# Optimization experiments

Measured on AMD Instinct MI355X. Metric: run time of the kernel, lower is better.

The kernel has to match this reference:

```python
import jax, jax.numpy as jnp
from jax import lax
import numpy as np

VOCAB, EMB, HID = 32000, 512, 512
START, STOP = 1, 2
B, T = 32, 32


def setup_inputs() -> dict:
    key = jax.random.key(0)
    ks = jax.random.split(key, 9)
    s = 0.02
    return {
        "x": jax.random.normal(ks[0], (B, HID), jnp.float32),
        "labels": jax.random.randint(ks[1], (B, T), 0, VOCAB),
        "coin": jax.random.randint(ks[2], (B, T), 0, 2).astype(bool),
        "emb": jax.random.normal(ks[3], (VOCAB, EMB), jnp.float32) * s,
        "Wi": jax.random.normal(ks[4], (EMB, 4 * HID), jnp.float32) * s,
        "Wh": jax.random.normal(ks[5], (HID, 4 * HID), jnp.float32) * s,
        "b": jnp.zeros((4 * HID,), jnp.float32),
        "Wo": jax.random.normal(ks[6], (HID, VOCAB), jnp.float32) * s,
        "bo": jnp.zeros((VOCAB,), jnp.float32),
    }


def reference(x, labels, coin, emb, Wi, Wh, b, Wo, bo):
    Bsz, Tlen = labels.shape

    def cell(inp, hn, cn):
        # PyTorch LSTMCell gate order: i, f, g, o
        gates = inp @ Wi + hn @ Wh + b  # [B, 4H]
        i_, f_, g_, o_ = jnp.split(gates, 4, axis=-1)
        cn = jax.nn.sigmoid(f_) * cn + jax.nn.sigmoid(i_) * jnp.tanh(g_)
        hn = jax.nn.sigmoid(o_) * jnp.tanh(cn)
        out = hn @ Wo + bo  # [B, V] logits
        return out, hn, cn

    inp0 = jnp.broadcast_to(emb[START], (Bsz, emb.shape[1]))
    hn0 = x                       # init_states: hidden <- image feature
    cn0 = jnp.zeros_like(x)
    loss0 = jnp.zeros((), jnp.float32)

    def step(carry, t_in):
        inp, hn, cn, loss = carry
        label_t, coin_t = t_in    # [B], [B]
        out, hn, cn = cell(inp, hn, cn)
        logp = jax.nn.log_softmax(out, axis=-1)
        ce = -jnp.take_along_axis(logp, label_t[:, None], axis=1)[:, 0]
        loss = loss + ce.sum()
        pred = jnp.argmax(out, axis=-1)  # scheduled sampling
        next_tok = jnp.where(coin_t, pred, label_t)
        return (emb[next_tok], hn, cn, loss), None

    (inp, hn, cn, loss), _ = lax.scan(step, (inp0, hn0, cn0, loss0), (labels.T, coin.T))

    # final STOP step
    out, hn, cn = cell(inp, hn, cn)
    logp = jax.nn.log_softmax(out, axis=-1)
    loss = loss + (-logp[:, STOP]).sum()
    return loss / Bsz
```

## Files before the change

kernel.cpp:

```cpp
#include <hip/hip_runtime.h>
#include <math.h>

#define VOCABSZ 32000
#define EMBD 512
#define HIDD 512
#define BSZ 32
#define TLEN 32
#define G4 2048
#define NGRP 1000
#define NLB 250
#define PSTRIDE 8192
#define SW 256.0f
#define SH 16.0f
#define INV_SWH (1.0f / (SW * SH))

using bf16x8 = __attribute__((ext_vector_type(8))) short;
using f32x16 = __attribute__((ext_vector_type(16))) float;
typedef long long i64;

__device__ __forceinline__ float sigmoidf_(float x) { return 1.f / (1.f + expf(-x)); }
__device__ __forceinline__ unsigned short f2bf(float f) {
    unsigned u = __float_as_uint(f);
    return (unsigned short)((u + 0x7fffu + ((u >> 16) & 1u)) >> 16);
}
__device__ __forceinline__ unsigned char f2e4m3(float f) {
    unsigned u = __float_as_uint(f);
    unsigned s = (u >> 24) & 0x80u;
    int e = (int)((u >> 23) & 0xffu);
    unsigned m = u & 0x7fffffu;
    int ee = e - 120;
    if (ee >= 16) return (unsigned char)(s | 0x7E);
    if (ee <= 0) return (unsigned char)s;
    unsigned r = m + 0x7FFFFu + ((m >> 20) & 1u);
    if (r & 0x800000u) { ee += 1; r = 0; if (ee >= 16) return (unsigned char)(s | 0x7E); }
    unsigned mant = (r >> 20) & 7u;
    if (ee == 15 && mant == 7u) return (unsigned char)(s | 0x7E);
    return (unsigned char)(s | (unsigned)(ee << 3) | mant);
}

__global__ void init6_kernel(const float* __restrict__ x,
                             const void* __restrict__ coin,
                             float* __restrict__ cst,
                             unsigned short* __restrict__ hbf,
                             unsigned char* __restrict__ hf8,
                             float* __restrict__ ce_acc, int* __restrict__ flag) {
    __shared__ int s_f;
    int tid = threadIdx.x;
    if (tid == 0) s_f = 0;
    __syncthreads();
    if (tid < 256 && ((const unsigned int*)coin)[tid] > 1u) s_f = 1;
    __syncthreads();
    if (tid == 0) *flag = s_f;
    if (tid < 32) ce_acc[tid] = 0.f;
    for (int i = tid; i < BSZ * HIDD; i += blockDim.x) {
        float v = x[i];
        cst[i] = 0.f;
        hbf[i] = f2bf(v);
        hf8[i] = f2e4m3(v * SH);
    }
}

__global__ __launch_bounds__(256) void emb_prep_kernel(
    const float* __restrict__ emb, unsigned short* __restrict__ embbf) {
    size_t i8 = ((size_t)blockIdx.x * 256 + threadIdx.x) * 8;
    float4 a = *(const float4*)&emb[i8];
    float4 b = *(const float4*)&emb[i8 + 4];
    bf16x8 v;
    v[0] = (short)f2bf(a.x); v[1] = (short)f2bf(a.y);
    v[2] = (short)f2bf(a.z); v[3] = (short)f2bf(a.w);
    v[4] = (short)f2bf(b.x); v[5] = (short)f2bf(b.y);
    v[6] = (short)f2bf(b.z); v[7] = (short)f2bf(b.w);
    *(bf16x8*)&embbf[i8] = v;
}

__global__ __launch_bounds__(256) void wot8_prep_kernel(
    const float* __restrict__ Wo, i64* __restrict__ wot8) {
    __shared__ unsigned char s[512 * 32];
    int g = blockIdx.x;
    int tid = threadIdx.x;
    int col = tid & 31;
    int k0 = tid >> 5;
    for (int kk = k0; kk < 512; kk += 8)
        s[kk * 32 + col] = f2e4m3(Wo[(size_t)kk * VOCABSZ + g * 32 + col] * SW);
    __syncthreads();
    for (int f = tid; f < 2048; f += 256) {
        int kt = f >> 6, lane = f & 63;
        int kb = kt * 16 + ((lane >> 5) << 3);
        int c = lane & 31;
        union { unsigned char b[8]; i64 v; } u;
        #pragma unroll
        for (int j = 0; j < 8; ++j) u.b[j] = s[(kb + j) * 32 + c];
        wot8[(size_t)g * 2048 + f] = u.v;
    }
}

__global__ __launch_bounds__(256) void wcell_prep_kernel(
    const float* __restrict__ Wi, const float* __restrict__ Wh,
    unsigned short* __restrict__ wcell) {
    __shared__ unsigned short s[512 * 32];
    int cb = blockIdx.x >> 1;
    int half = blockIdx.x & 1;
    const float* Wsrc = half ? Wh : Wi;
    int tid = threadIdx.x;
    int lc = tid & 31;
    int gcol = (lc >> 3) * 512 + cb * 8 + (lc & 7);
    int k0 = tid >> 5;
    for (int kl = k0; kl < 512; kl += 8)
        s[kl * 32 + lc] = f2bf(Wsrc[(size_t)kl * G4 + gcol]);
    __syncthreads();
    bf16x8* out8 = (bf16x8*)wcell;
    for (int f = tid; f < 2048; f += 256) {
        int ktl = f >> 6, lane = f & 63;
        int kb = ktl * 16 + ((lane >> 5) << 3);
        int c = lane & 31;
        bf16x8 v;
        #pragma unroll
        for (int j = 0; j < 8; ++j) v[j] = (short)s[(kb + j) * 32 + c];
        out8[((size_t)cb * 64 + half * 32 + ktl) * 64 + lane] = v;
    }
}

__global__ __launch_bounds__(1024) void cell_mfma4_kernel(
    const float* __restrict__ emb, const unsigned short* __restrict__ embbf,
    const int* __restrict__ labels,
    const void* __restrict__ coin, const int* __restrict__ flag,
    const unsigned short* __restrict__ wcell, const float* __restrict__ bias,
    float* __restrict__ cst, unsigned short* __restrict__ hbf,
    unsigned char* __restrict__ hf8,
    const float* __restrict__ part, float* __restrict__ ce_acc, int t) {
    __shared__ float sg[16][32][32];
    __shared__ float st[32][33];
    __shared__ int s_tok[32];
    int tid = threadIdx.x;
    int cb = blockIdx.x;
    int lane = tid & 63, wv = tid >> 6;

    if (t == 0) {
        if (tid < 32) s_tok[tid] = 1;
    } else {
        int row = tid >> 5, slot = tid & 31;
        int tm1 = t - 1;
        float m = -3.0e38f; int mi = 0;
        for (int ib = slot; ib < NLB; ib += 32) {
            int e = row * 256 + ib;
            float pm = part[e];
            int pi = __float_as_int(part[2 * PSTRIDE + e]);
            if (pm > m || (pm == m && pi < mi)) { m = pm; mi = pi; }
        }
        #pragma unroll
        for (int d = 1; d < 32; d <<= 1) {
            float om = __shfl_xor(m, d);
            int omi = __shfl_xor(mi, d);
            if (om > m || (om == m && omi < mi)) { m = om; mi = omi; }
        }
        if (slot == 0) {
            int lab = labels[row * TLEN + tm1];
            int cn = (*flag) ? (int)((const unsigned char*)coin)[row * TLEN + tm1]
                             : ((const int*)coin)[row * TLEN + tm1];
            s_tok[row] = cn ? mi : lab;
        }
        if (cb == 0) {
            float M = -3.0e38f, S = 0.f, L = -INFINITY;
            for (int ib = slot; ib < NLB; ib += 32) {
                int e = row * 256 + ib;
                float pm = part[e], ps = part[PSTRIDE + e];
                float nM = fmaxf(M, pm);
                S = S * expf(M - nM) + ps * expf(pm - nM);
                M = nM;
                L = fmaxf(L, part[3 * PSTRIDE + e]);
            }
            #pragma unroll
            for (int d = 1; d < 32; d <<= 1) {
                float oM = __shfl_xor(M, d), oS = __shfl_xor(S, d);
                float nM = fmaxf(M, oM);
                S = S * expf(M - nM) + oS * expf(oM - nM);
                M = nM;
                L = fmaxf(L, __shfl_xor(L, d));
            }
            if (slot == 0) ce_acc[row] += (M + logf(S)) - L;
        }
    }
    __syncthreads();

    int r = lane & 31;
    int ksub = (lane >> 5) << 3;
    const bf16x8* wp = (const bf16x8*)wcell + ((size_t)cb * 64 + wv * 4) * 64 + lane;

    f32x16 acc = {};
    if (wv < 8) {
        int tok = s_tok[r];
        if (embbf) {
            const unsigned short* eb = embbf + (size_t)tok * EMBD;
            #pragma unroll
            for (int i = 0; i < 4; ++i) {
                int k = (wv * 4 + i) * 16 + ksub;
                bf16x8 a = *(const bf16x8*)&eb[k];
                acc = __builtin_amdgcn_mfma_f32_32x32x16_bf16(a, wp[i * 64], acc, 0, 0, 0);
            }
        } else {
            const float* ebase = emb + (size_t)tok * EMBD;
            #pragma unroll
            for (int i = 0; i < 4; ++i) {
                int k = (wv * 4 + i) * 16 + ksub;
                float4 e0 = *(const float4*)(ebase + k);
                float4 e1 = *(const float4*)(ebase + k + 4);
                bf16x8 a;
                a[0] = (short)f2bf(e0.x); a[1] = (short)f2bf(e0.y);
                a[2] = (short)f2bf(e0.z); a[3] = (short)f2bf(e0.w);
                a[4] = (short)f2bf(e1.x); a[5] = (short)f2bf(e1.y);
                a[6] = (short)f2bf(e1.z); a[7] = (short)f2bf(e1.w);
                acc = __builtin_amdgcn_mfma_f32_32x32x16_bf16(a, wp[i * 64], acc, 0, 0, 0);
            }
        }
    } else {
        #pragma unroll
        for (int i = 0; i < 4; ++i) {
            int k = (wv * 4 + i) * 16 + ksub - 512;
            bf16x8 a = *(const bf16x8*)&hbf[r * HIDD + k];
            acc = __builtin_amdgcn_mfma_f32_32x32x16_bf16(a, wp[i * 64], acc, 0, 0, 0);
        }
    }

    int half = lane >> 5;
    #pragma unroll
    for (int reg = 0; reg < 16; ++reg) {
        int row = (reg & 3) + 8 * (reg >> 2) + 4 * half;
        sg[wv][row][lane & 31] = acc[reg];
    }
    __syncthreads();

    {
        int row = tid >> 5, lc = tid & 31;
        float s = 0.f;
        #pragma unroll
        for (int w = 0; w < 16; ++w) s += sg[w][row][lc];
        st[row][lc] = s;
    }
    __syncthreads();

    if (tid < 256) {
        int rr = tid >> 3, jj = tid & 7;
        int jh = cb * 8 + jj;
        float i_ = bias[jh]        + st[rr][jj];
        float f_ = bias[jh + 512]  + st[rr][jj + 8];
        float g_ = bias[jh + 1024] + st[rr][jj + 16];
        float o_ = bias[jh + 1536] + st[rr][jj + 24];
        int idx = rr * HIDD + jh;
        float ci = cst[idx];
        float cn = sigmoidf_(f_) * ci + sigmoidf_(i_) * tanhf(g_);
        float hn = sigmoidf_(o_) * tanhf(cn);
        cst[idx] = cn;
        hbf[idx] = f2bf(hn);
        hf8[idx] = f2e4m3(hn * SH);
    }
}

__global__ __launch_bounds__(256) void logits_fp8_kernel(
    const i64* __restrict__ wot8, const unsigned char* __restrict__ h_f8,
    const float* __restrict__ bo, const int* __restrict__ labels,
    float* __restrict__ part, int t) {
    __shared__ __align__(16) i64 s_h[2048];
    __shared__ int s_lab[32];
    __shared__ float s_pm[4][32], s_ps[4][32], s_pl[4][32], s_pst[4][32];
    __shared__ int s_pi[4][32];
    int tid = threadIdx.x;
    int lane = tid & 63, wv = tid >> 6;

    for (int f = tid; f < 2048; f += 256) {
        int kt = f >> 6, ln = f & 63;
        int row = ln & 31, kb = kt * 16 + ((ln >> 5) << 3);
        s_h[f] = *(const i64*)&h_f8[row * 512 + kb];
    }
    if (tid < 32) s_lab[tid] = labels[tid * TLEN + t];
    __syncthreads();

    int g = blockIdx.x * 4 + wv;
    const i64* wp = wot8 + (size_t)g * 2048 + lane;

    f32x16 acc0 = {}, acc1 = {};
    #pragma unroll 4
    for (int kt = 0; kt < 16; ++kt) {
        acc0 = __builtin_amdgcn_mfma_f32_32x32x16_fp8_fp8(
            s_h[kt * 64 + lane], wp[kt * 64], acc0, 0, 0, 0);
        acc1 = __builtin_amdgcn_mfma_f32_32x32x16_fp8_fp8(
            s_h[(kt + 16) * 64 + lane], wp[(kt + 16) * 64], acc1, 0, 0, 0);
    }

    int half = lane >> 5;
    int colw = lane & 31;
    int col = g * 32 + colw;
    float bq = bo[col];

    #pragma unroll
    for (int reg = 0; reg < 16; ++reg) {
        int row = (reg & 3) + 8 * (reg >> 2) + 4 * half;
        float v = (acc0[reg] + acc1[reg]) * INV_SWH + bq;
        float m = v; int mi = col;
        #pragma unroll
        for (int d = 1; d < 32; d <<= 1) {
            float om = __shfl_xor(m, d);
            int omi = __shfl_xor(mi, d);
            if (om > m || (om == m && omi < mi)) { m = om; mi = omi; }
        }
        float e = expf(v - m), ssum = e;
        #pragma unroll
        for (int d = 1; d < 32; d <<= 1) ssum += __shfl_xor(ssum, d);
        int labc = s_lab[row];
        float lv = __shfl(v, (labc & 31) + (half << 5));
        if ((labc >> 5) != g) lv = -INFINITY;
        float sv = __shfl(v, 2 + (half << 5));
        if (g != 0) sv = -INFINITY;
        if (colw == 0) {
            s_pm[wv][row] = m; s_ps[wv][row] = ssum; s_pi[wv][row] = mi;
            s_pl[wv][row] = lv; s_pst[wv][row] = sv;
        }
    }
    __syncthreads();

    if (tid < 32) {
        int row = tid;
        float M = s_pm[0][row], S = s_ps[0][row];
        int MI = s_pi[0][row];
        float L = s_pl[0][row], ST = s_pst[0][row];
        #pragma unroll
        for (int w = 1; w < 4; ++w) {
            float pm = s_pm[w][row], ps = s_ps[w][row];
            int pi = s_pi[w][row];
            float nM = fmaxf(M, pm);
            S = S * expf(M - nM) + ps * expf(pm - nM);
            if (pm > M || (pm == M && pi < MI)) MI = pi;
            M = nM;
            L = fmaxf(L, s_pl[w][row]);
            ST = fmaxf(ST, s_pst[w][row]);
        }
        int e0 = row * 256 + blockIdx.x;
        part[e0] = M;
        part[PSTRIDE + e0] = S;
        part[2 * PSTRIDE + e0] = __int_as_float(MI);
        part[3 * PSTRIDE + e0] = L;
        part[4 * PSTRIDE + e0] = ST;
    }
}

__global__ __launch_bounds__(256) void finalize5_kernel(
    const float* __restrict__ part, const float* __restrict__ ce_acc,
    float* __restrict__ out) {
    __shared__ float s_ce[32];
    int tid = threadIdx.x;
    int row = tid >> 3, slot = tid & 7;
    float M = -3.0e38f, S = 0.f, ST = -INFINITY;
    for (int ib = slot; ib < NLB; ib += 8) {
        int e = row * 256 + ib;
        float pm = part[e], ps = part[PSTRIDE + e];
        float nM = fmaxf(M, pm);
        S = S * expf(M - nM) + ps * expf(pm - nM);
        M = nM;
        ST = fmaxf(ST, part[4 * PSTRIDE + e]);
    }
    #pragma unroll
    for (int d = 1; d < 8; d <<= 1) {
        float oM = __shfl_xor(M, d), oS = __shfl_xor(S, d);
        float nM = fmaxf(M, oM);
        S = S * expf(M - nM) + oS * expf(oM - nM);
        M = nM;
        ST = fmaxf(ST, __shfl_xor(ST, d));
    }
    if (slot == 0) s_ce[row] = ce_acc[row] + (M + logf(S)) - ST;
    __syncthreads();
    if (tid == 0) {
        float tot = 0.f;
        for (int r = 0; r < 32; ++r) tot += s_ce[r];
        *out = tot / 32.f;
    }
}

extern "C" void kernel_launch(void* const* d_in, const int* in_sizes, int n_in,
                              void* d_out, int out_size, void* d_ws, size_t ws_size,
                              hipStream_t stream) {
    const float* x      = (const float*)d_in[0];
    const int*   labels = (const int*)  d_in[1];
    const void*  coin   =               d_in[2];
    const float* emb    = (const float*)d_in[3];
    const float* Wi     = (const float*)d_in[4];
    const float* Wh     = (const float*)d_in[5];
    const float* b      = (const float*)d_in[6];
    const float* Wo     = (const float*)d_in[7];
    const float* bo     = (const float*)d_in[8];

    float* ws     = (float*)d_ws;
    float* cst    = ws;
    unsigned short* h_bf = (unsigned short*)(ws + 16384);
    unsigned char*  h_f8 = (unsigned char*)(ws + 24576);
    float* part   = ws + 28672;
    float* ce_acc = ws + 69632;
    int*   flag   = (int*)(ws + 69664);
    unsigned short* wcell = (unsigned short*)(ws + 69696);
    i64*   wot8   = (i64*)(ws + 69696 + 1048576);
    unsigned short* embbf = (unsigned short*)(ws + 69696 + 1048576 + 4096000);
    float* outp   = (float*)d_out;

    size_t need_emb = (size_t)(69696 + 1048576 + 4096000 + 8192000) * 4;
    const unsigned short* embbf_use = (ws_size >= need_emb) ? embbf : (const unsigned short*)0;

    wot8_prep_kernel<<<NGRP, 256, 0, stream>>>(Wo, wot8);
    wcell_prep_kernel<<<128, 256, 0, stream>>>(Wi, Wh, wcell);
    if (embbf_use)
        emb_prep_kernel<<<VOCABSZ * EMBD / 2048, 256, 0, stream>>>(emb, embbf);
    init6_kernel<<<1, 256, 0, stream>>>(x, coin, cst, h_bf, h_f8, ce_acc, flag);

    for (int t = 0; t < 33; ++t) {
        int tt = (t < 32) ? t : 0;
        cell_mfma4_kernel<<<64, 1024, 0, stream>>>(emb, embbf_use, labels, coin,
                                                   flag, wcell, b, cst, h_bf,
                                                   h_f8, part, ce_acc, t);
        logits_fp8_kernel<<<NLB, 256, 0, stream>>>(wot8, h_f8, bo, labels,
                                                   part, tt);
    }
    finalize5_kernel<<<1, 256, 0, stream>>>(part, ce_acc, outp);
}
```

Measured before the change: 1.234 ms.

## Split logits K-reduction across two waves with 16-byte interleaved FP8 loads

The logits kernel now runs 512 threads per block, and two waves cover each 32-column group by splitting the K dimension in half. Partial accumulators from the second half pass through shared memory before the softmax/argmax reduction. Weights and hidden states are re-laid out so each lane loads two consecutive k-tiles with a single 16-byte load. The init kernel is also spread over 64 blocks instead of one. The aim is more waves in flight to hide memory latency on the weight stream, at the cost of an extra LDS round-trip and barrier.

```diff
diff --git a/kernel.cpp b/kernel.cpp
--- a/kernel.cpp
+++ b/kernel.cpp
@@ -38,26 +38,26 @@
     return (unsigned char)(s | (unsigned)(ee << 3) | mant);
 }
 
-__global__ void init6_kernel(const float* __restrict__ x,
-                             const void* __restrict__ coin,
-                             float* __restrict__ cst,
-                             unsigned short* __restrict__ hbf,
-                             unsigned char* __restrict__ hf8,
-                             float* __restrict__ ce_acc, int* __restrict__ flag) {
+__global__ __launch_bounds__(256) void init7_kernel(
+    const float* __restrict__ x, const void* __restrict__ coin,
+    float* __restrict__ cst, unsigned short* __restrict__ hbf,
+    unsigned char* __restrict__ hf8,
+    float* __restrict__ ce_acc, int* __restrict__ flag) {
     __shared__ int s_f;
     int tid = threadIdx.x;
-    if (tid == 0) s_f = 0;
-    __syncthreads();
-    if (tid < 256 && ((const unsigned int*)coin)[tid] > 1u) s_f = 1;
-    __syncthreads();
-    if (tid == 0) *flag = s_f;
-    if (tid < 32) ce_acc[tid] = 0.f;
-    for (int i = tid; i < BSZ * HIDD; i += blockDim.x) {
-        float v = x[i];
-        cst[i] = 0.f;
-        hbf[i] = f2bf(v);
-        hf8[i] = f2e4m3(v * SH);
-    }
+    int i = blockIdx.x * 256 + tid;
+    if (blockIdx.x == 0) {
+        if (tid == 0) s_f = 0;
+        __syncthreads();
+        if (((const unsigned int*)coin)[tid] > 1u) s_f = 1;
+        __syncthreads();
+        if (tid == 0) *flag = s_f;
+        if (tid < 32) ce_acc[tid] = 0.f;
+    }
+    float v = x[i];
+    cst[i] = 0.f;
+    hbf[i] = f2bf(v);
+    hf8[i] = f2e4m3(v * SH);
 }
 
 __global__ __launch_bounds__(256) void emb_prep_kernel(
@@ -90,7 +90,7 @@
         union { unsigned char b[8]; i64 v; } u;
         #pragma unroll
         for (int j = 0; j < 8; ++j) u.b[j] = s[(kb + j) * 32 + c];
-        wot8[(size_t)g * 2048 + f] = u.v;
+        wot8[(size_t)g * 2048 + (kt >> 1) * 128 + lane * 2 + (kt & 1)] = u.v;
     }
 }
 
@@ -255,64 +255,78 @@
     }
 }
 
-__global__ __launch_bounds__(256) void logits_fp8_kernel(
+__global__ __launch_bounds__(512, 4) void logits_fp8b_kernel(
     const i64* __restrict__ wot8, const unsigned char* __restrict__ h_f8,
     const float* __restrict__ bo, const int* __restrict__ labels,
     float* __restrict__ part, int t) {
     __shared__ __align__(16) i64 s_h[2048];
+    __shared__ float sacc[4][64][17];
     __shared__ int s_lab[32];
     __shared__ float s_pm[4][32], s_ps[4][32], s_pl[4][32], s_pst[4][32];
     __shared__ int s_pi[4][32];
     int tid = threadIdx.x;
     int lane = tid & 63, wv = tid >> 6;
-
-    for (int f = tid; f < 2048; f += 256) {
+    int p = wv & 3, kh = wv >> 2;
+
+    for (int f = tid; f < 2048; f += 512) {
         int kt = f >> 6, ln = f & 63;
         int row = ln & 31, kb = kt * 16 + ((ln >> 5) << 3);
-        s_h[f] = *(const i64*)&h_f8[row * 512 + kb];
+        s_h[(kt >> 1) * 128 + ln * 2 + (kt & 1)] = *(const i64*)&h_f8[row * 512 + kb];
     }
     if (tid < 32) s_lab[tid] = labels[tid * TLEN + t];
     __syncthreads();
 
-    int g = blockIdx.x * 4 + wv;
-    const i64* wp = wot8 + (size_t)g * 2048 + lane;
+    int g = blockIdx.x * 4 + p;
+    const ulonglong2* wp16 = (const ulonglong2*)(wot8 + (size_t)g * 2048) + lane;
+    const ulonglong2* sh16 = (const ulonglong2*)s_h + lane;
 
     f32x16 acc0 = {}, acc1 = {};
-    #pragma unroll 4
-    for (int kt = 0; kt < 16; ++kt) {
+    #pragma unroll
+    for (int i = 0; i < 8; ++i) {
+        int ktp = kh * 8 + i;
+        ulonglong2 ah = sh16[ktp * 64];
+        ulonglong2 wq = wp16[ktp * 64];
         acc0 = __builtin_amdgcn_mfma_f32_32x32x16_fp8_fp8(
-            s_h[kt * 64 + lane], wp[kt * 64], acc0, 0, 0, 0);
+            (i64)ah.x, (i64)wq.x, acc0, 0, 0, 0);
         acc1 = __builtin_amdgcn_mfma_f32_32x32x16_fp8_fp8(
-            s_h[(kt + 16) * 64 + lane], wp[(kt + 16) * 64], acc1, 0, 0, 0);
-    }
-
-    int half = lane >> 5;
-    int colw = lane & 31;
-    int col = g * 32 + colw;
-    float bq = bo[col];
-
-    #pragma unroll
-    for (int reg = 0; reg < 16; ++reg) {
-        int row = (reg & 3) + 8 * (reg >> 2) + 4 * half;
-        float v = (acc0[reg] + acc1[reg]) * INV_SWH + bq;
-        float m = v; int mi = col;
-        #pragma unroll
-        for (int d = 1; d < 32; d <<= 1) {
-            float om = __shfl_xor(m, d);
-            int omi = __shfl_xor(mi, d);
-            if (om > m || (om == m && omi < mi)) { m = om; mi = omi; }
-        }
-        float e = expf(v - m), ssum = e;
-        #pragma unroll
-        for (int d = 1; d < 32; d <<= 1) ssum += __shfl_xor(ssum, d);
-        int labc = s_lab[row];
-        float lv = __shfl(v, (labc & 31) + (half << 5));
-        if ((labc >> 5) != g) lv = -INFINITY;
-        float sv = __shfl(v, 2 + (half << 5));
-        if (g != 0) sv = -INFINITY;
-        if (colw == 0) {
-            s_pm[wv][row] = m; s_ps[wv][row] = ssum; s_pi[wv][row] = mi;
-            s_pl[wv][row] = lv; s_pst[wv][row] = sv;
+            (i64)ah.y, (i64)wq.y, acc1, 0, 0, 0);
+    }
+
+    if (kh == 1) {
+        #pragma unroll
+        for (int reg = 0; reg < 16; ++reg)
+            sacc[p][lane][reg] = acc0[reg] + acc1[reg];
+    }
+    __syncthreads();
+
+    if (kh == 0) {
+        int half = lane >> 5;
+        int colw = lane & 31;
+        int col = g * 32 + colw;
+        float bq = bo[col];
+        #pragma unroll
+        for (int reg = 0; reg < 16; ++reg) {
+            int row = (reg & 3) + 8 * (reg >> 2) + 4 * half;
+            float v = (acc0[reg] + acc1[reg] + sacc[p][lane][reg]) * INV_SWH + bq;
+            float m = v; int mi = col;
+            #pragma unroll
+            for (int d = 1; d < 32; d <<= 1) {
+                float om = __shfl_xor(m, d);
+                int omi = __shfl_xor(mi, d);
+                if (om > m || (om == m && omi < mi)) { m = om; mi = omi; }
+            }
+            float e = expf(v - m), ssum = e;
+            #pragma unroll
+            for (int d = 1; d < 32; d <<= 1) ssum += __shfl_xor(ssum, d);
+            int labc = s_lab[row];
+            float lv = __shfl(v, (labc & 31) + (half << 5));
+            if ((labc >> 5) != g) lv = -INFINITY;
+            float sv = __shfl(v, 2 + (half << 5));
+            if (g != 0) sv = -INFINITY;
+            if (colw == 0) {
+                s_pm[p][row] = m; s_ps[p][row] = ssum; s_pi[p][row] = mi;
+                s_pl[p][row] = lv; s_pst[p][row] = sv;
+            }
         }
     }
     __syncthreads();
@@ -406,15 +420,15 @@
     wcell_prep_kernel<<<128, 256, 0, stream>>>(Wi, Wh, wcell);
     if (embbf_use)
         emb_prep_kernel<<<VOCABSZ * EMBD / 2048, 256, 0, stream>>>(emb, embbf);
-    init6_kernel<<<1, 256, 0, stream>>>(x, coin, cst, h_bf, h_f8, ce_acc, flag);
+    init7_kernel<<<64, 256, 0, stream>>>(x, coin, cst, h_bf, h_f8, ce_acc, flag);
 
     for (int t = 0; t < 33; ++t) {
         int tt = (t < 32) ? t : 0;
         cell_mfma4_kernel<<<64, 1024, 0, stream>>>(emb, embbf_use, labels, coin,
                                                    flag, wcell, b, cst, h_bf,
                                                    h_f8, part, ce_acc, t);
-        logits_fp8_kernel<<<NLB, 256, 0, stream>>>(wot8, h_f8, bo, labels,
-                                                   part, tt);
+        logits_fp8b_kernel<<<NLB, 512, 0, stream>>>(wot8, h_f8, bo, labels,
+                                                    part, tt);
     }
     finalize5_kernel<<<1, 256, 0, stream>>>(part, ce_acc, outp);
 }
```

New measurement: 1.072 ms. -13.1%, faster.
